# Optimization experiments

Hardware: AMD Instinct MI355X
Metric: run time of the kernel (lower is better)

## Reference

```python
import jax, jax.numpy as jnp
import numpy as np
import math

PERCENT = 0.5

def setup_inputs() -> dict:
    key = jax.random.key(0)
    x = jax.random.normal(key, (32, 128, 112, 112), dtype=jnp.float32)
    return {"x": x}

def reference(x):
    # x: [B, C, H, W]; per-pixel top-k over channels, keep values >= k-th largest, clamp at 0
    C = x.shape[1]
    k = math.ceil(PERCENT * C)
    xt = jnp.moveaxis(x, 1, -1)                 # [B, H, W, C]
    top_vals, _ = jax.lax.top_k(xt, k)          # [B, H, W, k]
    threshold = top_vals[..., -1:]              # k-th largest per pixel
    out = jnp.where(xt >= threshold, xt, jnp.float32(0.0))
    out = jnp.maximum(out, jnp.float32(0.0))    # clamp(min=0)
    return jnp.moveaxis(out, -1, 1)             # back to [B, C, H, W]
```

## Files before the change

kernel.cpp:

```cpp
#include <hip/hip_runtime.h>


#define CC   128
#define HWSZ 12544

__device__ __forceinline__ void bitonic64(float v[64]) {
  #pragma unroll
  for (int k = 2; k <= 64; k <<= 1) {
    #pragma unroll
    for (int j = k >> 1; j > 0; j >>= 1) {
      #pragma unroll
      for (int i = 0; i < 64; ++i) {
        int l = i ^ j;
        if (l > i) {
          float lo = fminf(v[i], v[l]);
          float hi = fmaxf(v[i], v[l]);
          bool up = ((i & k) == 0);
          v[i] = up ? lo : hi;
          v[l] = up ? hi : lo;
        }
      }
    }
  }
}

__global__ __launch_bounds__(256) void crelu_pct_kernel(
    const float* __restrict__ x, float* __restrict__ out) {
  const int t    = blockIdx.x * blockDim.x + threadIdx.x;
  const int q    = t >> 1;
  const int half = t & 1;
  const int n = q / HWSZ;
  const int p = q - n * HWSZ;
  const size_t base = (size_t)n * ((size_t)CC * HWSZ) + (size_t)p
                    + (size_t)(half << 6) * HWSZ;
  const float* xp = x + base;
  float*       op = out + base;

  float v[64];
  #pragma unroll
  for (int c = 0; c < 64; ++c) v[c] = xp[(size_t)c * HWSZ];
  bitonic64(v);

  float thr;
  {
    float mine  = half ? v[63] : v[0];
    float other = __shfl_xor(mine, 1, 64);
    thr = fmaxf(mine, other);
    #pragma unroll
    for (int i = 1; i < 64; ++i) {
      float m  = half ? v[63 - i] : v[i];
      float o  = __shfl_xor(m, 1, 64);
      thr = fminf(thr, fmaxf(m, o));
    }
  }

  #pragma unroll
  for (int c = 0; c < 64; ++c) {
    float w = xp[(size_t)c * HWSZ];
    op[(size_t)c * HWSZ] = (w >= thr && w > 0.0f) ? w : 0.0f;
  }
}

extern "C" void kernel_launch(void* const* d_in, const int* in_sizes, int n_in,
                              void* d_out, int out_size, void* d_ws, size_t ws_size,
                              hipStream_t stream) {
  const float* x = (const float*)d_in[0];
  float* out = (float*)d_out;
  const int npix = in_sizes[0] / CC;
  const int nthreads = npix * 2;
  const int block = 256;
  const int grid = nthreads / block;
  crelu_pct_kernel<<<grid, block, 0, stream>>>(x, out);
}
```

Baseline: 364.3 us.

## Stage thresholds in LDS and rewrite output pass with float4 nontemporal stores

Blocks now cover 128 contiguous pixels within one image. Each thread pair computes its pixel's threshold and writes it to shared memory. The second pass is rewritten so each thread re-reads four adjacent pixels per channel as float4 vectors and writes them with nontemporal stores. The goal is wider global accesses and less cache pollution from the large output stream, at the cost of a block barrier and a layout remap between the two passes.

```diff
diff --git a/kernel.cpp b/kernel.cpp
--- a/kernel.cpp
+++ b/kernel.cpp
@@ -1,8 +1,12 @@
 #include <hip/hip_runtime.h>
 
 
-#define CC   128
-#define HWSZ 12544
+#define CC        128
+#define HWSZ      12544
+#define PBLK      128
+#define NBLK_PER_N 98
+
+using f32x4 = __attribute__((ext_vector_type(4))) float;
 
 __device__ __forceinline__ void bitonic64(float v[64]) {
   #pragma unroll
@@ -26,15 +30,18 @@
 
 __global__ __launch_bounds__(256) void crelu_pct_kernel(
     const float* __restrict__ x, float* __restrict__ out) {
-  const int t    = blockIdx.x * blockDim.x + threadIdx.x;
-  const int q    = t >> 1;
-  const int half = t & 1;
-  const int n = q / HWSZ;
-  const int p = q - n * HWSZ;
-  const size_t base = (size_t)n * ((size_t)CC * HWSZ) + (size_t)p
-                    + (size_t)(half << 6) * HWSZ;
-  const float* xp = x + base;
-  float*       op = out + base;
+  __shared__ __align__(16) float thr_lds[PBLK];
+
+  const int tid = threadIdx.x;
+  const int n   = blockIdx.x / NBLK_PER_N;
+  const int pb  = (blockIdx.x - n * NBLK_PER_N) * PBLK;
+
+  const int ql   = tid >> 1;
+  const int half = tid & 1;
+  const size_t planeN = (size_t)CC * HWSZ;
+  const float* xp = x + (size_t)n * planeN
+                      + (size_t)(half << 6) * HWSZ
+                      + (size_t)(pb + ql);
 
   float v[64];
   #pragma unroll
@@ -48,16 +55,34 @@
     thr = fmaxf(mine, other);
     #pragma unroll
     for (int i = 1; i < 64; ++i) {
-      float m  = half ? v[63 - i] : v[i];
-      float o  = __shfl_xor(m, 1, 64);
+      float m = half ? v[63 - i] : v[i];
+      float o = __shfl_xor(m, 1, 64);
       thr = fminf(thr, fmaxf(m, o));
     }
   }
+  if (!half) thr_lds[ql] = thr;
+  __syncthreads();
 
+  const int j  = tid & 31;
+  const int c0 = tid >> 5;
+  const f32x4 t4 = *reinterpret_cast<const f32x4*>(&thr_lds[j << 2]);
+  const size_t rowpix = (size_t)n * planeN + (size_t)pb + (size_t)(j << 2);
+
+  f32x4 w[16];
   #pragma unroll
-  for (int c = 0; c < 64; ++c) {
-    float w = xp[(size_t)c * HWSZ];
-    op[(size_t)c * HWSZ] = (w >= thr && w > 0.0f) ? w : 0.0f;
+  for (int i = 0; i < 16; ++i) {
+    const int c = (i << 3) + c0;
+    w[i] = *reinterpret_cast<const f32x4*>(x + rowpix + (size_t)c * HWSZ);
+  }
+  #pragma unroll
+  for (int i = 0; i < 16; ++i) {
+    const int c = (i << 3) + c0;
+    f32x4 r;
+    #pragma unroll
+    for (int e = 0; e < 4; ++e)
+      r[e] = (w[i][e] >= t4[e] && w[i][e] > 0.0f) ? w[i][e] : 0.0f;
+    __builtin_nontemporal_store(
+        r, reinterpret_cast<f32x4*>(out + rowpix + (size_t)c * HWSZ));
   }
 }
 
@@ -67,8 +92,6 @@
   const float* x = (const float*)d_in[0];
   float* out = (float*)d_out;
   const int npix = in_sizes[0] / CC;
-  const int nthreads = npix * 2;
-  const int block = 256;
-  const int grid = nthreads / block;
-  crelu_pct_kernel<<<grid, block, 0, stream>>>(x, out);
+  const int grid = npix / PBLK;
+  crelu_pct_kernel<<<grid, 256, 0, stream>>>(x, out);
 }
```

Measured after the change: 354.4 us. 2.7% less time.
